# Optimization experiments

Hardware: AMD Instinct MI355X
Metric: run time of the kernel (lower is better)

## Reference

```python
import jax, jax.numpy as jnp
import numpy as np

D_MODEL = 1024
NHEAD = 16
HEAD_DIM = D_MODEL // NHEAD
D_FF = 4096
B, S = 2, 2048
LN_EPS = 1e-5


def _linear_params(key, d_out, d_in):
    kw, kb = jax.random.split(key)
    lim = 1.0 / np.sqrt(d_in)
    W = jax.random.uniform(kw, (d_out, d_in), jnp.float32, -lim, lim)
    b = jax.random.uniform(kb, (d_out,), jnp.float32, -lim, lim)
    return W, b


def setup_inputs() -> dict:
    key = jax.random.key(0)
    ks = jax.random.split(key, 8)
    src = jax.random.normal(ks[0], (B, S, D_MODEL), jnp.float32)
    mask = jax.random.randint(ks[1], (B, S), 0, 2).astype(bool)
    Wq, bq = _linear_params(ks[2], D_MODEL, D_MODEL)
    Wk, bk = _linear_params(ks[3], D_MODEL, D_MODEL)
    Wv, bv = _linear_params(ks[4], D_MODEL, D_MODEL)
    Wo, bo = _linear_params(ks[5], D_MODEL, D_MODEL)
    W1, b1 = _linear_params(ks[6], D_FF, D_MODEL)
    W2, b2 = _linear_params(ks[7], D_MODEL, D_FF)
    ln1_g = jnp.ones((D_MODEL,), jnp.float32)
    ln1_b = jnp.zeros((D_MODEL,), jnp.float32)
    ln2_g = jnp.ones((D_MODEL,), jnp.float32)
    ln2_b = jnp.zeros((D_MODEL,), jnp.float32)
    return dict(src=src, mask=mask, Wq=Wq, bq=bq, Wk=Wk, bk=bk, Wv=Wv, bv=bv,
                Wo=Wo, bo=bo, W1=W1, b1=b1, W2=W2, b2=b2,
                ln1_g=ln1_g, ln1_b=ln1_b, ln2_g=ln2_g, ln2_b=ln2_b)


def _layernorm(x, g, b):
    mu = jnp.mean(x, axis=-1, keepdims=True)
    var = jnp.mean(jnp.square(x - mu), axis=-1, keepdims=True)
    return (x - mu) * jax.lax.rsqrt(var + LN_EPS) * g + b


def reference(src, mask, Wq, bq, Wk, bk, Wv, bv, Wo, bo, W1, b1, W2, b2,
              ln1_g, ln1_b, ln2_g, ln2_b):
    batch, seq, _ = src.shape
    src_norm = _layernorm(src, ln1_g, ln1_b)
    # projections (torch Linear: x @ W.T + b), split heads -> [B,H,S,Dh]
    def proj(W, b):
        y = jnp.einsum('bsi,oi->bso', src_norm, W) + b
        return y.reshape(batch, seq, NHEAD, HEAD_DIM).transpose(0, 2, 1, 3)
    q, k, v = proj(Wq, bq), proj(Wk, bk), proj(Wv, bv)
    scores = jnp.einsum('bhqd,bhkd->bhqk', q, k) / np.sqrt(HEAD_DIM)
    scores = jnp.where(mask[:, None, None, :], -10000.0, scores)
    attn_probs = jax.nn.softmax(scores, axis=-1)
    attn_out = jnp.einsum('bhqk,bhkd->bhqd', attn_probs, v)
    attn_out = attn_out.transpose(0, 2, 1, 3).reshape(batch, seq, D_MODEL)
    attn_out = jnp.einsum('bsi,oi->bso', attn_out, Wo) + bo
    src = src + attn_out
    src_norm2 = _layernorm(src, ln2_g, ln2_b)
    h = jax.nn.relu(jnp.einsum('bsi,oi->bso', src_norm2, W1) + b1)
    ff = jnp.einsum('bsi,oi->bso', h, W2) + b2
    src = src + ff
    return (src, attn_probs)
```

## Files before the change

kernel.cpp:

```cpp
#include <hip/hip_runtime.h>
#include <math.h>

typedef __bf16 bf16;
typedef __bf16 bf16x4 __attribute__((ext_vector_type(4)));
typedef __bf16 bf16x8 __attribute__((ext_vector_type(8)));
typedef float f32x4 __attribute__((ext_vector_type(4)));

__device__ __forceinline__ f32x4 mfma16(bf16x8 a, bf16x8 b, f32x4 c) {
  return __builtin_amdgcn_mfma_f32_16x16x32_bf16(a, b, c, 0, 0, 0);
}

__device__ __forceinline__ void gload_lds16(const void* g, void* l) {
  __builtin_amdgcn_global_load_lds((__attribute__((address_space(1))) void*)(g),
                                   (__attribute__((address_space(3))) void*)(l),
                                   16, 0, 0);
}

__global__ void cvt_bf16(const float* __restrict__ in, bf16* __restrict__ out, int n4) {
  int i = blockIdx.x * blockDim.x + threadIdx.x;
  if (i >= n4) return;
  float4 v = reinterpret_cast<const float4*>(in)[i];
  bf16x4 o;
  o[0] = (bf16)v.x; o[1] = (bf16)v.y; o[2] = (bf16)v.z; o[3] = (bf16)v.w;
  reinterpret_cast<bf16x4*>(out)[i] = o;
}

__global__ void concat3(const float* __restrict__ a, const float* __restrict__ b,
                        const float* __restrict__ c, float* __restrict__ o) {
  int i = blockIdx.x * blockDim.x + threadIdx.x;
  if (i >= 3072) return;
  float v = (i < 1024) ? a[i] : ((i < 2048) ? b[i - 1024] : c[i - 2048]);
  o[i] = v;
}

__global__ __launch_bounds__(256)
void ln_bf16(const float* __restrict__ x, const float* __restrict__ g,
             const float* __restrict__ bta, bf16* __restrict__ y) {
  const int row = blockIdx.x, t = threadIdx.x;
  const float4 v = reinterpret_cast<const float4*>(x)[(size_t)row * 256 + t];
  float s1 = v.x + v.y + v.z + v.w;
  float s2 = v.x * v.x + v.y * v.y + v.z * v.z + v.w * v.w;
#pragma unroll
  for (int m = 1; m < 64; m <<= 1) {
    s1 += __shfl_xor(s1, m);
    s2 += __shfl_xor(s2, m);
  }
  __shared__ float red[8];
  if ((t & 63) == 0) { red[(t >> 6) * 2] = s1; red[(t >> 6) * 2 + 1] = s2; }
  __syncthreads();
  s1 = red[0] + red[2] + red[4] + red[6];
  s2 = red[1] + red[3] + red[5] + red[7];
  const float mu = s1 * (1.f / 1024.f);
  const float rs = rsqrtf(s2 * (1.f / 1024.f) - mu * mu + 1e-5f);
  const float4 gv = reinterpret_cast<const float4*>(g)[t];
  const float4 bv = reinterpret_cast<const float4*>(bta)[t];
  bf16x4 o;
  o[0] = (bf16)((v.x - mu) * rs * gv.x + bv.x);
  o[1] = (bf16)((v.y - mu) * rs * gv.y + bv.y);
  o[2] = (bf16)((v.z - mu) * rs * gv.z + bv.z);
  o[3] = (bf16)((v.w - mu) * rs * gv.w + bv.w);
  reinterpret_cast<bf16x4*>(y)[(size_t)row * 256 + t] = o;
}

__global__ __launch_bounds__(256)
void tr_v(const bf16* __restrict__ QKV, bf16* __restrict__ VT) {
  __shared__ bf16 T[64 * 80];
  const int t = threadIdx.x;
  const int sb = blockIdx.x * 64, h = blockIdx.y, b = blockIdx.z;
  const int srow = t >> 2, c16 = t & 3;
  const bf16* src = QKV + (size_t)(b * 2048 + sb + srow) * 3072 + 2048 + h * 64 + c16 * 16;
  bf16x8 a0 = *reinterpret_cast<const bf16x8*>(src);
  bf16x8 a1 = *reinterpret_cast<const bf16x8*>(src + 8);
  *reinterpret_cast<bf16x8*>(&T[srow * 80 + c16 * 16]) = a0;
  *reinterpret_cast<bf16x8*>(&T[srow * 80 + c16 * 16 + 8]) = a1;
  __syncthreads();
  const int drow = t >> 2, sq = t & 3;
  bf16x8 o0, o1;
#pragma unroll
  for (int j = 0; j < 8; ++j) o0[j] = T[(sq * 16 + j) * 80 + drow];
#pragma unroll
  for (int j = 0; j < 8; ++j) o1[j] = T[(sq * 16 + 8 + j) * 80 + drow];
  bf16* dst = VT + ((size_t)(b * 16 + h) * 64 + drow) * 2048 + sb + sq * 16;
  *reinterpret_cast<bf16x8*>(dst) = o0;
  *reinterpret_cast<bf16x8*>(dst + 8) = o1;
}

template <bool OUT_BF16, bool RELU, bool RES, bool QSC>
__global__ __launch_bounds__(256)
void gemm_bt(const bf16* __restrict__ A, const bf16* __restrict__ Bw,
             const float* __restrict__ bias, const float* __restrict__ res,
             void* __restrict__ Cout, int M, int N, int K) {
  __shared__ bf16 As[2][128 * 32];
  __shared__ bf16 Bs[2][128 * 32];
  const int t = threadIdx.x, wave = t >> 6, lane = t & 63;
  const int l15 = lane & 15, lhi = lane >> 4;
  const int nwg = gridDim.x * gridDim.y;
  const int orig = blockIdx.y * gridDim.x + blockIdx.x;
  const int wgid = (orig & 7) * (nwg >> 3) + (orig >> 3);
  const int bx = wgid % gridDim.x, by = wgid / gridDim.x;
  const int m0 = by * 128, n0 = bx * 128;
  const int wm = (wave >> 1) * 64, wn = (wave & 1) * 64;
  const f32x4 z4 = {0.f, 0.f, 0.f, 0.f};
  f32x4 acc[4][4];
#pragma unroll
  for (int m = 0; m < 4; ++m)
#pragma unroll
    for (int n = 0; n < 4; ++n) acc[m][n] = z4;

  const int soff0 = wave * 1024 + lane * 16;
  const int soff1 = (4 + wave) * 1024 + lane * 16;
  const int srow0 = soff0 >> 6, scol0 = (soff0 & 63) >> 1;
  const int srow1 = soff1 >> 6, scol1 = (soff1 & 63) >> 1;

#define GEMM_STAGE(k0, bb)                                                    \
  do {                                                                        \
    gload_lds16(A + (size_t)(m0 + srow0) * K + (k0) + scol0,                  \
                (char*)As[bb] + soff0);                                       \
    gload_lds16(Bw + (size_t)(n0 + srow0) * K + (k0) + scol0,                 \
                (char*)Bs[bb] + soff0);                                       \
    gload_lds16(A + (size_t)(m0 + srow1) * K + (k0) + scol1,                  \
                (char*)As[bb] + soff1);                                       \
    gload_lds16(Bw + (size_t)(n0 + srow1) * K + (k0) + scol1,                 \
                (char*)Bs[bb] + soff1);                                       \
  } while (0)

  GEMM_STAGE(0, 0);
  asm volatile("s_waitcnt vmcnt(0)" ::: "memory");
  __builtin_amdgcn_s_barrier();

  int cur = 0;
  for (int k0 = 0; k0 < K; k0 += 32) {
    if (k0 + 32 < K) GEMM_STAGE(k0 + 32, cur ^ 1);
    bf16x8 af[4], bfr[4];
#pragma unroll
    for (int m = 0; m < 4; ++m)
      af[m] = *reinterpret_cast<const bf16x8*>(&As[cur][(wm + m * 16 + l15) * 32 + lhi * 8]);
#pragma unroll
    for (int n = 0; n < 4; ++n)
      bfr[n] = *reinterpret_cast<const bf16x8*>(&Bs[cur][(wn + n * 16 + l15) * 32 + lhi * 8]);
#pragma unroll
    for (int m = 0; m < 4; ++m)
#pragma unroll
      for (int n = 0; n < 4; ++n) acc[m][n] = mfma16(af[m], bfr[n], acc[m][n]);
    asm volatile("s_waitcnt vmcnt(0)" ::: "memory");
    __builtin_amdgcn_s_barrier();
    cur ^= 1;
  }
#undef GEMM_STAGE

  const float sc = (QSC && n0 < 1024) ? 0.125f : 1.0f;
#pragma unroll
  for (int m = 0; m < 4; ++m) {
    const int row_base = m0 + wm + m * 16 + lhi * 4;
#pragma unroll
    for (int n = 0; n < 4; ++n) {
      const int col = n0 + wn + n * 16 + l15;
      const float bv = bias[col];
#pragma unroll
      for (int r = 0; r < 4; ++r) {
        const int row = row_base + r;
        float v = (acc[m][n][r] + bv) * sc;
        if (RELU) v = v > 0.f ? v : 0.f;
        if (RES) v += res[(size_t)row * N + col];
        if (OUT_BF16)
          ((bf16*)Cout)[(size_t)row * N + col] = (bf16)v;
        else
          ((float*)Cout)[(size_t)row * N + col] = v;
      }
    }
  }
}

__global__ __launch_bounds__(256)
void attn_fused2(const bf16* __restrict__ Qp, const bf16* __restrict__ Kp,
                 const bf16* __restrict__ VTp, const int* __restrict__ mask,
                 float* __restrict__ probs, bf16* __restrict__ Ob) {
  constexpr int S = 2048, LD = 3072, KB = 128, NT = S / KB;
  __shared__ bf16 Kt[KB * 64];
  __shared__ bf16 Vt[64 * KB];
  __shared__ bf16 P[64 * KB];
  __shared__ float msk[KB];
  const int t = threadIdx.x, wave = t >> 6, lane = t & 63;
  const int l15 = lane & 15, lhi = lane >> 4;
  const int flat = blockIdx.x + 32 * (blockIdx.y + 16 * blockIdx.z);
  const int wg = (flat & 7) * 128 + (flat >> 3);
  const int q0 = (wg & 31) * 64, h = (wg >> 5) & 15, b = wg >> 9;
  const int* mrow = mask + b * S;
  const f32x4 z4 = {0.f, 0.f, 0.f, 0.f};

  bf16x8 qf[2];
#pragma unroll
  for (int ks = 0; ks < 2; ++ks)
    qf[ks] = *reinterpret_cast<const bf16x8*>(
        Qp + (size_t)(b * S + q0 + wave * 16 + l15) * LD + h * 64 + ks * 32 + lhi * 8);

  float lpart = 0.f;
  for (int kt = 0; kt < NT; ++kt) {
    const int kv0 = kt * KB;
#pragma unroll
    for (int i = 0; i < 4; ++i) {
      const int off = (i * 4 + wave) * 1024 + lane * 16;
      const int row = off >> 7, binr = off & 127;
      const int sb = binr ^ ((row & 7) << 4);
      gload_lds16(Kp + (size_t)(b * S + kv0 + row) * LD + h * 64 + (sb >> 1),
                  (char*)Kt + (i * 4 + wave) * 1024);
    }
    if (t < KB) msk[t] = mrow[kv0 + t] ? 0.f : 1.f;
    __syncthreads();
    f32x4 sa[8];
#pragma unroll
    for (int n = 0; n < 8; ++n) sa[n] = z4;
#pragma unroll
    for (int ks = 0; ks < 2; ++ks)
#pragma unroll
      for (int n = 0; n < 8; ++n) {
        const int krow = n * 16 + l15;
        bf16x8 kf = *reinterpret_cast<const bf16x8*>(
            (char*)Kt + krow * 128 + ((ks * 64 + lhi * 16) ^ ((krow & 7) << 4)));
        sa[n] = mfma16(kf, qf[ks], sa[n]);
      }
#pragma unroll
    for (int n = 0; n < 8; ++n)
#pragma unroll
      for (int r = 0; r < 4; ++r)
        lpart += __expf(sa[n][r] - 15.f) * msk[n * 16 + lhi * 4 + r];
    __syncthreads();
  }
  lpart += __shfl_xor(lpart, 16);
  lpart += __shfl_xor(lpart, 32);
  const float il = 1.f / lpart;

  f32x4 oa[4];
#pragma unroll
  for (int n = 0; n < 4; ++n) oa[n] = z4;
  float* pbase = probs + ((size_t)(b * 16 + h) * S + q0 + wave * 16 + l15) * S;
  const int prw = wave * 16 + l15;

  for (int kt = 0; kt < NT; ++kt) {
    const int kv0 = kt * KB;
#pragma unroll
    for (int i = 0; i < 4; ++i) {
      const int off = (i * 4 + wave) * 1024 + lane * 16;
      const int row = off >> 7, binr = off & 127;
      const int sb = binr ^ ((row & 7) << 4);
      gload_lds16(Kp + (size_t)(b * S + kv0 + row) * LD + h * 64 + (sb >> 1),
                  (char*)Kt + (i * 4 + wave) * 1024);
    }
#pragma unroll
    for (int i = 0; i < 4; ++i) {
      const int off = (i * 4 + wave) * 1024 + lane * 16;
      const int d = off >> 8, binb = off & 255;
      const int sb = binb ^ ((d & 7) << 4);
      gload_lds16(VTp + (size_t)((b * 16 + h) * 64 + d) * S + kv0 + (sb >> 1),
                  (char*)Vt + (i * 4 + wave) * 1024);
    }
    if (t < KB) msk[t] = mrow[kv0 + t] ? 0.f : 1.f;
    __syncthreads();

    f32x4 sa[8];
#pragma unroll
    for (int n = 0; n < 8; ++n) sa[n] = z4;
#pragma unroll
    for (int ks = 0; ks < 2; ++ks)
#pragma unroll
      for (int n = 0; n < 8; ++n) {
        const int krow = n * 16 + l15;
        bf16x8 kf = *reinterpret_cast<const bf16x8*>(
            (char*)Kt + krow * 128 + ((ks * 64 + lhi * 16) ^ ((krow & 7) << 4)));
        sa[n] = mfma16(kf, qf[ks], sa[n]);
      }

#pragma unroll
    for (int n = 0; n < 8; ++n) {
      f32x4 pn;
#pragma unroll
      for (int r = 0; r < 4; ++r)
        pn[r] = __expf(sa[n][r] - 15.f) * msk[n * 16 + lhi * 4 + r] * il;
      *reinterpret_cast<f32x4*>(pbase + kv0 + n * 16 + lhi * 4) = pn;
      bf16x4 pb;
      pb[0] = (bf16)pn[0]; pb[1] = (bf16)pn[1];
      pb[2] = (bf16)pn[2]; pb[3] = (bf16)pn[3];
      *reinterpret_cast<bf16x4*>(
          (char*)P + prw * 256 + ((n * 32 + lhi * 8) ^ ((prw & 7) << 4))) = pb;
    }
#pragma unroll
    for (int ks = 0; ks < 4; ++ks) {
      bf16x8 pf = *reinterpret_cast<const bf16x8*>(
          (char*)P + prw * 256 + ((ks * 64 + lhi * 16) ^ ((prw & 7) << 4)));
#pragma unroll
      for (int nn = 0; nn < 4; ++nn) {
        const int vr = nn * 16 + l15;
        bf16x8 vf = *reinterpret_cast<const bf16x8*>(
            (char*)Vt + vr * 256 + ((ks * 64 + lhi * 16) ^ ((vr & 7) << 4)));
        oa[nn] = mfma16(pf, vf, oa[nn]);
      }
    }
    __syncthreads();
  }

#pragma unroll
  for (int nn = 0; nn < 4; ++nn)
#pragma unroll
    for (int r = 0; r < 4; ++r)
      Ob[(size_t)(b * S + q0 + wave * 16 + lhi * 4 + r) * 1024 + h * 64 + nn * 16 + l15] =
          (bf16)oa[nn][r];
}

extern "C" void kernel_launch(void* const* d_in, const int* in_sizes, int n_in,
                              void* d_out, int out_size, void* d_ws, size_t ws_size,
                              hipStream_t stream) {
  const float* src = (const float*)d_in[0];
  const int* mask = (const int*)d_in[1];
  const float* Wq = (const float*)d_in[2];
  const float* bq = (const float*)d_in[3];
  const float* Wk = (const float*)d_in[4];
  const float* bk = (const float*)d_in[5];
  const float* Wv = (const float*)d_in[6];
  const float* bv = (const float*)d_in[7];
  const float* Wo = (const float*)d_in[8];
  const float* bo = (const float*)d_in[9];
  const float* W1 = (const float*)d_in[10];
  const float* b1 = (const float*)d_in[11];
  const float* W2 = (const float*)d_in[12];
  const float* b2 = (const float*)d_in[13];
  const float* ln1g = (const float*)d_in[14];
  const float* ln1b = (const float*)d_in[15];
  const float* ln2g = (const float*)d_in[16];
  const float* ln2b = (const float*)d_in[17];

  float* out0 = (float*)d_out;
  float* probs = (float*)d_out + (size_t)4194304;

  char* w = (char*)d_ws;
  const size_t MB = 1u << 20;
  bf16* wqkv = (bf16*)(w);
  bf16* wob = (bf16*)(w + 6 * MB);
  bf16* w1b = (bf16*)(w + 8 * MB);
  bf16* w2b = (bf16*)(w + 16 * MB);
  bf16* xn = (bf16*)(w + 24 * MB);
  bf16* QKV = (bf16*)(w + 32 * MB);
  bf16* Ob = (bf16*)(w + 56 * MB);
  bf16* hb = (bf16*)(w + 32 * MB);
  bf16* VT = (bf16*)(w + 64 * MB);
  float* s2 = (float*)(w + 64 * MB);
  float* bqkv = (float*)(w + 80 * MB);

  cvt_bf16<<<1024, 256, 0, stream>>>(Wq, wqkv, 262144);
  cvt_bf16<<<1024, 256, 0, stream>>>(Wk, wqkv + 1024 * 1024, 262144);
  cvt_bf16<<<1024, 256, 0, stream>>>(Wv, wqkv + 2 * 1024 * 1024, 262144);
  cvt_bf16<<<1024, 256, 0, stream>>>(Wo, wob, 262144);
  cvt_bf16<<<4096, 256, 0, stream>>>(W1, w1b, 1048576);
  cvt_bf16<<<4096, 256, 0, stream>>>(W2, w2b, 1048576);
  concat3<<<12, 256, 0, stream>>>(bq, bk, bv, bqkv);

  ln_bf16<<<4096, 256, 0, stream>>>(src, ln1g, ln1b, xn);
  gemm_bt<true, false, false, true><<<dim3(24, 32), 256, 0, stream>>>(
      xn, wqkv, bqkv, nullptr, QKV, 4096, 3072, 1024);
  tr_v<<<dim3(32, 16, 2), 256, 0, stream>>>(QKV, VT);
  attn_fused2<<<dim3(32, 16, 2), 256, 0, stream>>>(
      QKV, QKV + 1024, VT, mask, probs, Ob);
  gemm_bt<false, false, true, false><<<dim3(8, 32), 256, 0, stream>>>(
      Ob, wob, bo, src, s2, 4096, 1024, 1024);
  ln_bf16<<<4096, 256, 0, stream>>>(s2, ln2g, ln2b, xn);
  gemm_bt<true, true, false, false><<<dim3(32, 32), 256, 0, stream>>>(
      xn, w1b, b1, nullptr, hb, 4096, 4096, 1024);
  gemm_bt<false, false, true, false><<<dim3(8, 32), 256, 0, stream>>>(
      hb, w2b, b2, s2, out0, 4096, 1024, 4096);

  (void)in_sizes; (void)n_in; (void)out_size; (void)ws_size;
}
```

Measured before the change: 475.3 us.

## Register-prefetch next K/V tiles in attention and merge weight-conversion kernels

The attention kernel now loads the next K (and V) tile plus mask into registers while the current tile is computed, then writes them to LDS after a barrier. This replaces the direct global-to-LDS loads that stalled at the start of every tile. The seven weight and bias conversion launches are also merged into one kernel to cut launch overhead. The prefetch adds register pressure and an extra barrier per tile, which could lower occupancy.

```diff
diff --git a/kernel.cpp b/kernel.cpp
--- a/kernel.cpp
+++ b/kernel.cpp
@@ -16,21 +16,33 @@
                                    16, 0, 0);
 }
 
-__global__ void cvt_bf16(const float* __restrict__ in, bf16* __restrict__ out, int n4) {
-  int i = blockIdx.x * blockDim.x + threadIdx.x;
-  if (i >= n4) return;
-  float4 v = reinterpret_cast<const float4*>(in)[i];
-  bf16x4 o;
-  o[0] = (bf16)v.x; o[1] = (bf16)v.y; o[2] = (bf16)v.z; o[3] = (bf16)v.w;
-  reinterpret_cast<bf16x4*>(out)[i] = o;
-}
-
-__global__ void concat3(const float* __restrict__ a, const float* __restrict__ b,
-                        const float* __restrict__ c, float* __restrict__ o) {
-  int i = blockIdx.x * blockDim.x + threadIdx.x;
-  if (i >= 3072) return;
-  float v = (i < 1024) ? a[i] : ((i < 2048) ? b[i - 1024] : c[i - 2048]);
-  o[i] = v;
+__global__ __launch_bounds__(256)
+void cvt_all(const float* __restrict__ Wq, const float* __restrict__ Wk,
+             const float* __restrict__ Wv, const float* __restrict__ Wo,
+             const float* __restrict__ W1, const float* __restrict__ W2,
+             const float* __restrict__ bq, const float* __restrict__ bk,
+             const float* __restrict__ bv, bf16* __restrict__ wqkv,
+             bf16* __restrict__ wob, bf16* __restrict__ w1b,
+             bf16* __restrict__ w2b, float* __restrict__ bqkv) {
+  const int i = blockIdx.x * 256 + threadIdx.x;
+  if (i < 3145728) {
+    float4 v;
+    bf16* dst;
+    size_t di;
+    if (i < 262144) { v = ((const float4*)Wq)[i]; dst = wqkv; di = i; }
+    else if (i < 524288) { v = ((const float4*)Wk)[i - 262144]; dst = wqkv; di = i; }
+    else if (i < 786432) { v = ((const float4*)Wv)[i - 524288]; dst = wqkv; di = i; }
+    else if (i < 1048576) { v = ((const float4*)Wo)[i - 786432]; dst = wob; di = i - 786432; }
+    else if (i < 2097152) { v = ((const float4*)W1)[i - 1048576]; dst = w1b; di = i - 1048576; }
+    else { v = ((const float4*)W2)[i - 2097152]; dst = w2b; di = i - 2097152; }
+    bf16x4 o;
+    o[0] = (bf16)v.x; o[1] = (bf16)v.y; o[2] = (bf16)v.z; o[3] = (bf16)v.w;
+    reinterpret_cast<bf16x4*>(dst)[di] = o;
+  } else {
+    const int j = i - 3145728;
+    const float* s = (j < 256) ? bq : ((j < 512) ? bk : bv);
+    reinterpret_cast<float4*>(bqkv)[j] = reinterpret_cast<const float4*>(s)[j & 255];
+  }
 }
 
 __global__ __launch_bounds__(256)
@@ -188,25 +200,45 @@
   const int* mrow = mask + b * S;
   const f32x4 z4 = {0.f, 0.f, 0.f, 0.f};
 
+  const bf16* kgp[4];
+  const bf16* vgp[4];
+  int soff[4];
+#pragma unroll
+  for (int i = 0; i < 4; ++i) {
+    const int off = (i * 4 + wave) * 1024 + lane * 16;
+    soff[i] = off;
+    const int krow = off >> 7, kbin = off & 127;
+    kgp[i] = Kp + (size_t)(b * S + krow) * LD + h * 64 + ((kbin ^ ((krow & 7) << 4)) >> 1);
+    const int d = off >> 8, vbin = off & 255;
+    vgp[i] = VTp + (size_t)((b * 16 + h) * 64 + d) * S + ((vbin ^ ((d & 7) << 4)) >> 1);
+  }
+
   bf16x8 qf[2];
 #pragma unroll
   for (int ks = 0; ks < 2; ++ks)
     qf[ks] = *reinterpret_cast<const bf16x8*>(
         Qp + (size_t)(b * S + q0 + wave * 16 + l15) * LD + h * 64 + ks * 32 + lhi * 8);
 
+  bf16x8 kreg[4];
+  float mnext;
+#pragma unroll
+  for (int i = 0; i < 4; ++i) kreg[i] = *reinterpret_cast<const bf16x8*>(kgp[i]);
+  mnext = (t < KB) ? (mrow[t] ? 0.f : 1.f) : 0.f;
+#pragma unroll
+  for (int i = 0; i < 4; ++i)
+    *reinterpret_cast<bf16x8*>((char*)Kt + soff[i]) = kreg[i];
+  if (t < KB) msk[t] = mnext;
+  __syncthreads();
+
   float lpart = 0.f;
   for (int kt = 0; kt < NT; ++kt) {
     const int kv0 = kt * KB;
-#pragma unroll
-    for (int i = 0; i < 4; ++i) {
-      const int off = (i * 4 + wave) * 1024 + lane * 16;
-      const int row = off >> 7, binr = off & 127;
-      const int sb = binr ^ ((row & 7) << 4);
-      gload_lds16(Kp + (size_t)(b * S + kv0 + row) * LD + h * 64 + (sb >> 1),
-                  (char*)Kt + (i * 4 + wave) * 1024);
-    }
-    if (t < KB) msk[t] = mrow[kv0 + t] ? 0.f : 1.f;
-    __syncthreads();
+    if (kt + 1 < NT) {
+#pragma unroll
+      for (int i = 0; i < 4; ++i)
+        kreg[i] = *reinterpret_cast<const bf16x8*>(kgp[i] + (size_t)(kv0 + KB) * LD);
+      mnext = (t < KB) ? (mrow[kv0 + KB + t] ? 0.f : 1.f) : 0.f;
+    }
     f32x4 sa[8];
 #pragma unroll
     for (int n = 0; n < 8; ++n) sa[n] = z4;
@@ -225,6 +257,13 @@
       for (int r = 0; r < 4; ++r)
         lpart += __expf(sa[n][r] - 15.f) * msk[n * 16 + lhi * 4 + r];
     __syncthreads();
+    if (kt + 1 < NT) {
+#pragma unroll
+      for (int i = 0; i < 4; ++i)
+        *reinterpret_cast<bf16x8*>((char*)Kt + soff[i]) = kreg[i];
+      if (t < KB) msk[t] = mnext;
+    }
+    __syncthreads();
   }
   lpart += __shfl_xor(lpart, 16);
   lpart += __shfl_xor(lpart, 32);
@@ -236,26 +275,31 @@
   float* pbase = probs + ((size_t)(b * 16 + h) * S + q0 + wave * 16 + l15) * S;
   const int prw = wave * 16 + l15;
 
+  bf16x8 vreg[4];
+#pragma unroll
+  for (int i = 0; i < 4; ++i) {
+    kreg[i] = *reinterpret_cast<const bf16x8*>(kgp[i]);
+    vreg[i] = *reinterpret_cast<const bf16x8*>(vgp[i]);
+  }
+  mnext = (t < KB) ? (mrow[t] ? 0.f : 1.f) : 0.f;
+#pragma unroll
+  for (int i = 0; i < 4; ++i) {
+    *reinterpret_cast<bf16x8*>((char*)Kt + soff[i]) = kreg[i];
+    *reinterpret_cast<bf16x8*>((char*)Vt + soff[i]) = vreg[i];
+  }
+  if (t < KB) msk[t] = mnext;
+  __syncthreads();
+
   for (int kt = 0; kt < NT; ++kt) {
     const int kv0 = kt * KB;
-#pragma unroll
-    for (int i = 0; i < 4; ++i) {
-      const int off = (i * 4 + wave) * 1024 + lane * 16;
-      const int row = off >> 7, binr = off & 127;
-      const int sb = binr ^ ((row & 7) << 4);
-      gload_lds16(Kp + (size_t)(b * S + kv0 + row) * LD + h * 64 + (sb >> 1),
-                  (char*)Kt + (i * 4 + wave) * 1024);
-    }
-#pragma unroll
-    for (int i = 0; i < 4; ++i) {
-      const int off = (i * 4 + wave) * 1024 + lane * 16;
-      const int d = off >> 8, binb = off & 255;
-      const int sb = binb ^ ((d & 7) << 4);
-      gload_lds16(VTp + (size_t)((b * 16 + h) * 64 + d) * S + kv0 + (sb >> 1),
-                  (char*)Vt + (i * 4 + wave) * 1024);
-    }
-    if (t < KB) msk[t] = mrow[kv0 + t] ? 0.f : 1.f;
-    __syncthreads();
+    if (kt + 1 < NT) {
+#pragma unroll
+      for (int i = 0; i < 4; ++i) {
+        kreg[i] = *reinterpret_cast<const bf16x8*>(kgp[i] + (size_t)(kv0 + KB) * LD);
+        vreg[i] = *reinterpret_cast<const bf16x8*>(vgp[i] + kv0 + KB);
+      }
+      mnext = (t < KB) ? (mrow[kv0 + KB + t] ? 0.f : 1.f) : 0.f;
+    }
 
     f32x4 sa[8];
 #pragma unroll
@@ -294,6 +338,15 @@
             (char*)Vt + vr * 256 + ((ks * 64 + lhi * 16) ^ ((vr & 7) << 4)));
         oa[nn] = mfma16(pf, vf, oa[nn]);
       }
+    }
+    __syncthreads();
+    if (kt + 1 < NT) {
+#pragma unroll
+      for (int i = 0; i < 4; ++i) {
+        *reinterpret_cast<bf16x8*>((char*)Kt + soff[i]) = kreg[i];
+        *reinterpret_cast<bf16x8*>((char*)Vt + soff[i]) = vreg[i];
+      }
+      if (t < KB) msk[t] = mnext;
     }
     __syncthreads();
   }
@@ -345,13 +398,8 @@
   float* s2 = (float*)(w + 64 * MB);
   float* bqkv = (float*)(w + 80 * MB);
 
-  cvt_bf16<<<1024, 256, 0, stream>>>(Wq, wqkv, 262144);
-  cvt_bf16<<<1024, 256, 0, stream>>>(Wk, wqkv + 1024 * 1024, 262144);
-  cvt_bf16<<<1024, 256, 0, stream>>>(Wv, wqkv + 2 * 1024 * 1024, 262144);
-  cvt_bf16<<<1024, 256, 0, stream>>>(Wo, wob, 262144);
-  cvt_bf16<<<4096, 256, 0, stream>>>(W1, w1b, 1048576);
-  cvt_bf16<<<4096, 256, 0, stream>>>(W2, w2b, 1048576);
-  concat3<<<12, 256, 0, stream>>>(bq, bk, bv, bqkv);
+  cvt_all<<<12291, 256, 0, stream>>>(Wq, Wk, Wv, Wo, W1, W2, bq, bk, bv,
+                                     wqkv, wob, w1b, w2b, bqkv);
 
   ln_bf16<<<4096, 256, 0, stream>>>(src, ln1g, ln1b, xn);
   gemm_bt<true, false, false, true><<<dim3(24, 32), 256, 0, stream>>>(
```

Result: faster. 450.9 us (-5.1%).
